# Performance work log

Measured on AMD Instinct MI355X. Metric: run time of the kernel, lower is better.

## Reference

```python
import jax, jax.numpy as jnp
import numpy as np

D_MODEL = 1024
NHEAD = 16
HEAD_DIM = D_MODEL // NHEAD
MASK_FILLER = -1e20


def setup_inputs() -> dict:
    key = jax.random.key(0)
    ks = jax.random.split(key, 8)
    B, S = 2, 2048
    query = jax.random.normal(ks[0], (B, S, D_MODEL), dtype=jnp.float32)
    key_t = jax.random.normal(ks[1], (B, S, D_MODEL), dtype=jnp.float32)
    value = jax.random.normal(ks[2], (B, S, D_MODEL), dtype=jnp.float32)
    mask = jax.random.randint(ks[3], (B, S, S), 0, 2, dtype=jnp.int32)
    # nn.Linear(d_model, d_model, bias=False) weights, shape [out, in]
    scale = 1.0 / np.sqrt(D_MODEL)
    wq = jax.random.uniform(ks[4], (D_MODEL, D_MODEL), jnp.float32, -scale, scale)
    wk = jax.random.uniform(ks[5], (D_MODEL, D_MODEL), jnp.float32, -scale, scale)
    wv = jax.random.uniform(ks[6], (D_MODEL, D_MODEL), jnp.float32, -scale, scale)
    wo = jax.random.uniform(ks[7], (D_MODEL, D_MODEL), jnp.float32, -scale, scale)
    return {"query": query, "key": key_t, "value": value, "mask": mask,
            "wq": wq, "wk": wk, "wv": wv, "wo": wo}


def reference(query, key, value, mask, wq, wk, wv, wo):
    B = query.shape[0]
    # Projections: nn.Linear -> x @ W.T
    q = (query @ wq.T).reshape(B, -1, NHEAD, HEAD_DIM).transpose(0, 2, 1, 3)  # [B,H,Sq,Dh]
    k = (key @ wk.T).reshape(B, -1, NHEAD, HEAD_DIM).transpose(0, 2, 1, 3)    # [B,H,Sk,Dh]
    v = (value @ wv.T).reshape(B, -1, NHEAD, HEAD_DIM).transpose(0, 2, 1, 3)  # [B,H,Sk,Dh]
    scores = jnp.einsum('bhqd,bhkd->bhqk', q, k) / jnp.sqrt(jnp.float32(HEAD_DIM))
    scores = jnp.where(mask[:, None, :, :] == 0, MASK_FILLER, scores)
    attn = jax.nn.softmax(scores, axis=-1)  # dropout p=0.0 -> identity
    out = jnp.einsum('bhqk,bhkd->bhqd', attn, v)  # [B,H,Sq,Dh]
    out = out.transpose(0, 2, 1, 3).reshape(B, -1, D_MODEL)
    return out @ wo.T
```

## Files before the change

### kernel.cpp

```cpp
#include <hip/hip_runtime.h>
#include <stdint.h>

typedef __bf16 bf16x8 __attribute__((ext_vector_type(8)));
typedef __bf16 bf16x4 __attribute__((ext_vector_type(4)));
typedef float floatx4 __attribute__((ext_vector_type(4)));
typedef unsigned short ushort8v __attribute__((ext_vector_type(8)));
typedef unsigned int uint4v __attribute__((ext_vector_type(4)));
typedef unsigned int uint2v __attribute__((ext_vector_type(2)));
typedef unsigned short u16;
typedef unsigned long long u64;

#define GLOAD_LDS16(gp, lp)                                                       \
  __builtin_amdgcn_global_load_lds((__attribute__((address_space(1))) void*)(gp), \
                                   (__attribute__((address_space(3))) void*)(lp), \
                                   16, 0, 0)

__device__ __forceinline__ u16 f2bf(float f) {
  uint32_t u = __builtin_bit_cast(uint32_t, f);
  u = (u + 0x7FFFu + ((u >> 16) & 1u)) >> 16;
  return (u16)u;
}

__device__ __forceinline__ ushort8v load8(const void* base, size_t elemOff, int isf32) {
  if (isf32) {
    const uint32_t* p = (const uint32_t*)base + elemOff;
    uint4v a = *(const uint4v*)p;
    uint4v b = *(const uint4v*)(p + 4);
#pragma unroll
    for (int i = 0; i < 4; ++i) { a[i] += 0x8000u; b[i] += 0x8000u; }
    uint4v r;
    r[0] = __builtin_amdgcn_perm(a[1], a[0], 0x07060302);
    r[1] = __builtin_amdgcn_perm(a[3], a[2], 0x07060302);
    r[2] = __builtin_amdgcn_perm(b[1], b[0], 0x07060302);
    r[3] = __builtin_amdgcn_perm(b[3], b[2], 0x07060302);
    return __builtin_bit_cast(ushort8v, r);
  }
  return *(const ushort8v*)((const u16*)base + elemOff);
}

__global__ void detect_dtype(const u16* __restrict__ q, int* __restrict__ flag) {
  if (threadIdx.x == 0) *flag = 0;
  __syncthreads();
  int hit = 0;
  for (int i = threadIdx.x; i < 8192; i += 256) {
    u16 u = q[i];
    if (((u >> 7) & 0xFF) == 0xFF) hit = 1;
  }
  if (hit) atomicOr(flag, 1);
}

__global__ void pack_mask(const int* __restrict__ mask, u64* __restrict__ mpk) {
  const int gw   = (blockIdx.x * 256 + threadIdx.x) >> 6;
  const int lane = threadIdx.x & 63;
  const int word = gw & 31;
  const int row  = gw >> 5;
  const int m = mask[(size_t)row * 2048 + word * 64 + lane];
  u64 bits = __ballot(m != 0);
  if (lane == 0) mpk[(size_t)row * 32 + word] = bits;
}

__global__ __launch_bounds__(256)
void cvt_all(const void* X0, const void* X1, const void* X2,
             const void* W0, const void* W1, const void* W2, const void* W3,
             u16* __restrict__ Xb, u16* __restrict__ Wb, const int* flagp)
{
  const int isf = *flagp;
  const int id = blockIdx.x;
  const int t  = threadIdx.x;
  const int r2  = t >> 7;
  const int col = (t & 127) * 8;
  const void* src; u16* dst; int row;
  if (id < 6144) {
    const int s = id >> 11;
    src = (s == 0) ? X0 : (s == 1) ? X1 : X2;
    row = (id & 2047) * 2 + r2;
    dst = Xb + (size_t)s * 4096 * 1040 + (size_t)row * 1040 + col;
  } else {
    const int s = (id - 6144) >> 9;
    src = (s == 0) ? W0 : (s == 1) ? W1 : (s == 2) ? W2 : W3;
    row = ((id - 6144) & 511) * 2 + r2;
    dst = Wb + (size_t)s * 1024 * 1040 + (size_t)row * 1040 + col;
  }
  *(ushort8v*)dst = load8(src, (size_t)row * 1024 + col, isf);
}

__global__ __launch_bounds__(256)
void cvt_w(const void* W0, const void* W1, const void* W2, const void* W3,
           u16* __restrict__ dst, const int* flagp) {
  const int isf = *flagp;
  const int z = blockIdx.y;
  const void* src = (z == 0) ? W0 : (z == 1) ? W1 : (z == 2) ? W2 : W3;
  const size_t off = ((size_t)blockIdx.x * 256 + threadIdx.x) * 8;
  *(ushort8v*)(dst + (size_t)z * 1024 * 1024 + off) = load8(src, off, isf);
}

__global__ __launch_bounds__(256, 3)
void gemm_qkv_b(const u16* __restrict__ Xb, const u16* __restrict__ Wb,
                u16* __restrict__ Qb, u16* __restrict__ Kb, u16* __restrict__ Vt)
{
  const int AS = 1040, WS = 1040, N = 1024, K = 1024;
  const int z = blockIdx.z;
  const u16* A = Xb + (size_t)z * 4096 * AS;
  const u16* W = Wb + (size_t)z * 1024 * WS;

  __shared__ __align__(16) u16 lA[2 * 128 * 32];
  __shared__ __align__(16) u16 lB[2 * 128 * 32];

  const int tid  = threadIdx.x;
  const int lane = tid & 63;
  const int quad = lane >> 4;
  const int l15  = lane & 15;
  const int w    = tid >> 6;
  const int wm   = w >> 1, wn = w & 1;
  const int tileM = blockIdx.x * 128;
  const int tileN = blockIdx.y * 128;

  floatx4 acc[4][4] = {};

  const int ldRow = tid >> 2;
  const int ldCol = (tid & 3) * 8;
  const u16* aG = A + (size_t)(tileM + ldRow) * AS + ldCol;
  const u16* bG = W + (size_t)(tileN + ldRow) * WS + ldCol;
  u16* lAp = lA + tid * 8;
  u16* lBp = lB + tid * 8;

  GLOAD_LDS16(aG, lAp);
  GLOAD_LDS16(aG + (size_t)64 * AS, lAp + 2048);
  GLOAD_LDS16(bG, lBp);
  GLOAD_LDS16(bG + (size_t)64 * WS, lBp + 2048);
  __syncthreads();

#pragma unroll 2
  for (int k0 = 0; k0 < K; k0 += 32) {
    const int cur = (k0 >> 5) & 1;
    const int nxo = 4096 * (cur ^ 1);
    if (k0 + 32 < K) {
      GLOAD_LDS16(aG + k0 + 32, lAp + nxo);
      GLOAD_LDS16(aG + (size_t)64 * AS + k0 + 32, lAp + nxo + 2048);
      GLOAD_LDS16(bG + k0 + 32, lBp + nxo);
      GLOAD_LDS16(bG + (size_t)64 * WS + k0 + 32, lBp + nxo + 2048);
    }
    const u16* cA = lA + 4096 * cur;
    const u16* cB = lB + 4096 * cur;
    bf16x8 af[4], bw[4];
#pragma unroll
    for (int i = 0; i < 4; ++i) {
      af[i] = *(const bf16x8*)&cA[(wm * 64 + i * 16 + l15) * 32 + quad * 8];
      bw[i] = *(const bf16x8*)&cB[(wn * 64 + i * 16 + l15) * 32 + quad * 8];
    }
#pragma unroll
    for (int i = 0; i < 4; ++i)
#pragma unroll
      for (int j = 0; j < 4; ++j)
        acc[i][j] = __builtin_amdgcn_mfma_f32_16x16x32_bf16(af[i], bw[j], acc[i][j], 0, 0, 0);
    __syncthreads();
  }

  if (z < 2) {
    u16* C = (z == 0) ? Qb : Kb;
    const float sc = (z == 0) ? 0.18033688011112042f : 1.0f;
#pragma unroll
    for (int i = 0; i < 4; ++i) {
      const int row0 = tileM + wm * 64 + i * 16 + quad * 4;
#pragma unroll
      for (int j = 0; j < 4; ++j) {
        const int col = tileN + wn * 64 + j * 16 + l15;
#pragma unroll
        for (int r = 0; r < 4; ++r)
          C[(size_t)(row0 + r) * N + col] = f2bf(acc[i][j][r] * sc);
      }
    }
  } else {
    const int half = w >> 1;
    u16* myT = (w & 1) ? lB : lA;
#pragma unroll
    for (int pass = 0; pass < 2; ++pass) {
      __syncthreads();
      if (half == pass) {
#pragma unroll
        for (int i = 0; i < 4; ++i)
#pragma unroll
          for (int j = 0; j < 4; ++j)
#pragma unroll
            for (int r = 0; r < 4; ++r) {
              const int lr = i * 16 + quad * 4 + r;
              const int lc = j * 16 + l15;
              myT[lr * 64 + (lc ^ (quad << 4))] = f2bf(acc[i][j][r]);
            }
      }
      __syncthreads();
      if (half == pass) {
        const int n    = lane;
        const int gcol = tileN + wn * 64 + n;
        const int hh = gcol >> 6, dd = gcol & 63;
        const int growBase = tileM + wm * 64;
        const int bb = growBase >> 11;
        const int s0 = growBase & 2047;
        u16* dst = Vt + (((size_t)bb * 16 + hh) * 64 + dd) * 2048 + s0;
#pragma unroll
        for (int m0 = 0; m0 < 64; m0 += 8) {
          ushort8v pk;
#pragma unroll
          for (int t = 0; t < 8; ++t) {
            const int m = m0 + t;
            pk[t] = myT[m * 64 + (n ^ ((m & 12) << 2))];
          }
          *(ushort8v*)(dst + m0) = pk;
        }
      }
    }
  }
}

__global__ __launch_bounds__(256)
void gemm_qkv_f(const void* X0, const void* X1, const void* X2,
                const u16* __restrict__ Wb,
                u16* __restrict__ Qb, u16* __restrict__ Kb, u16* __restrict__ Vt,
                const int* flagp)
{
  const int K = 1024, N = 1024;
  const int isf = *flagp;
  const int z = blockIdx.z;
  const void* A_ = (z == 0) ? X0 : (z == 1) ? X1 : X2;
  const u16* W = Wb + (size_t)z * 1024 * 1024;

  __shared__ __align__(16) u16 lA[128 * 32];
  __shared__ __align__(16) u16 lB[128 * 32];

  const int tid  = threadIdx.x;
  const int lane = tid & 63;
  const int quad = lane >> 4;
  const int l15  = lane & 15;
  const int w    = tid >> 6;
  const int wm   = w >> 1, wn = w & 1;
  const int tileM = blockIdx.x * 128;
  const int tileN = blockIdx.y * 128;

  floatx4 acc[4][4] = {};

  const int ldRow = tid >> 2;
  const int ldCol = (tid & 3) * 8;
  const size_t aOff = (size_t)(tileM + ldRow) * K + ldCol;
  const u16* bG = W + (size_t)(tileN + ldRow) * K + ldCol;
  u16* lAp = lA + tid * 8;
  u16* lBp = lB + tid * 8;

  ushort8v a0 = load8(A_, aOff, isf);
  ushort8v a1 = load8(A_, aOff + (size_t)64 * K, isf);
  ushort8v b0 = *(const ushort8v*)bG;
  ushort8v b1 = *(const ushort8v*)(bG + (size_t)64 * K);

  for (int k0 = 0; k0 < K; k0 += 32) {
    __syncthreads();
    *(ushort8v*)lAp          = a0;
    *(ushort8v*)(lAp + 2048) = a1;
    *(ushort8v*)lBp          = b0;
    *(ushort8v*)(lBp + 2048) = b1;
    __syncthreads();

    if (k0 + 32 < K) {
      a0 = load8(A_, aOff + k0 + 32, isf);
      a1 = load8(A_, aOff + (size_t)64 * K + k0 + 32, isf);
      b0 = *(const ushort8v*)(bG + k0 + 32);
      b1 = *(const ushort8v*)(bG + (size_t)64 * K + k0 + 32);
    }

    bf16x8 af[4], bw[4];
#pragma unroll
    for (int i = 0; i < 4; ++i) {
      af[i] = *(const bf16x8*)&lA[(wm * 64 + i * 16 + l15) * 32 + quad * 8];
      bw[i] = *(const bf16x8*)&lB[(wn * 64 + i * 16 + l15) * 32 + quad * 8];
    }
#pragma unroll
    for (int i = 0; i < 4; ++i)
#pragma unroll
      for (int j = 0; j < 4; ++j)
        acc[i][j] = __builtin_amdgcn_mfma_f32_16x16x32_bf16(af[i], bw[j], acc[i][j], 0, 0, 0);
  }

  if (z < 2) {
    u16* C = (z == 0) ? Qb : Kb;
    const float sc = (z == 0) ? 0.18033688011112042f : 1.0f;
#pragma unroll
    for (int i = 0; i < 4; ++i) {
      const int row0 = tileM + wm * 64 + i * 16 + quad * 4;
#pragma unroll
      for (int j = 0; j < 4; ++j) {
        const int col = tileN + wn * 64 + j * 16 + l15;
#pragma unroll
        for (int r = 0; r < 4; ++r)
          C[(size_t)(row0 + r) * N + col] = f2bf(acc[i][j][r] * sc);
      }
    }
  } else {
    const int half = w >> 1;
    u16* myT = (w & 1) ? lB : lA;
#pragma unroll
    for (int pass = 0; pass < 2; ++pass) {
      __syncthreads();
      if (half == pass) {
#pragma unroll
        for (int i = 0; i < 4; ++i)
#pragma unroll
          for (int j = 0; j < 4; ++j)
#pragma unroll
            for (int r = 0; r < 4; ++r) {
              const int lr = i * 16 + quad * 4 + r;
              const int lc = j * 16 + l15;
              myT[lr * 64 + (lc ^ (quad << 4))] = f2bf(acc[i][j][r]);
            }
      }
      __syncthreads();
      if (half == pass) {
        const int n    = lane;
        const int gcol = tileN + wn * 64 + n;
        const int hh = gcol >> 6, dd = gcol & 63;
        const int growBase = tileM + wm * 64;
        const int bb = growBase >> 11;
        const int s0 = growBase & 2047;
        u16* dst = Vt + (((size_t)bb * 16 + hh) * 64 + dd) * 2048 + s0;
#pragma unroll
        for (int m0 = 0; m0 < 64; m0 += 8) {
          ushort8v pk;
#pragma unroll
          for (int t = 0; t < 8; ++t) {
            const int m = m0 + t;
            pk[t] = myT[m * 64 + (n ^ ((m & 12) << 2))];
          }
          *(ushort8v*)(dst + m0) = pk;
        }
      }
    }
  }
}

__global__ __launch_bounds__(256)
void attn(const u16* Qb, const u16* __restrict__ Kb, const u16* __restrict__ Vt,
          const u64* __restrict__ mpk, u16* AO, int aoStr)
{
  __shared__ __align__(16) u16 lK[2][64 * 64];
  __shared__ __align__(16) u16 lV[2][64 * 64];
  __shared__ __align__(16) u16 lP[4][16 * 64];

  const int tid  = threadIdx.x;
  const int lane = tid & 63;
  const int quad = lane >> 4;
  const int l15  = lane & 15;
  const int w    = tid >> 6;

  const int bh = blockIdx.x;
  const int qt = blockIdx.y;
  const int b  = bh >> 4;
  const int h  = bh & 15;
  const size_t rowB   = (size_t)b * 2048;
  const size_t vtBase = ((size_t)bh * 64) * 2048;

  bf16x8 aq[2];
  {
    const u16* qp = Qb + (rowB + qt * 64 + w * 16 + l15) * 1024 + h * 64 + quad * 8;
    aq[0] = *(const bf16x8*)qp;
    aq[1] = *(const bf16x8*)(qp + 32);
  }

  const ushort8v one_u = {0x3F80, 0x3F80, 0x3F80, 0x3F80, 0x3F80, 0x3F80, 0x3F80, 0x3F80};
  const bf16x8 ones = __builtin_bit_cast(bf16x8, one_u);

  floatx4 o[4], l4;
#pragma unroll
  for (int nb = 0; nb < 4; ++nb) o[nb] = (floatx4){0.f, 0.f, 0.f, 0.f};
  l4 = (floatx4){0.f, 0.f, 0.f, 0.f};

  const u64* mrow = mpk + (rowB + qt * 64 + w * 16 + l15) * 32;
  u16* lPw = &lP[w][0];

  const int r1 = tid >> 3;
  const int cs = ((tid & 7) ^ (r1 & 7)) * 8;
  const u16* kSrc = Kb + (rowB + r1) * 1024 + h * 64 + cs;
  const u16* vSrc = Vt + vtBase + (size_t)r1 * 2048 + cs;

  GLOAD_LDS16(kSrc,                     &lK[0][tid * 8]);
  GLOAD_LDS16(kSrc + (size_t)32 * 1024, &lK[0][tid * 8 + 2048]);
  GLOAD_LDS16(vSrc,                     &lV[0][tid * 8]);
  GLOAD_LDS16(vSrc + (size_t)32 * 2048, &lV[0][tid * 8 + 2048]);

#pragma unroll 2
  for (int kt = 0; kt < 32; ++kt) {
    const int cur = kt & 1;
    __syncthreads();
    if (kt < 31) {
      const u16* kS = kSrc + (size_t)(kt + 1) * 64 * 1024;
      const u16* vS = vSrc + (kt + 1) * 64;
      GLOAD_LDS16(kS,                     &lK[cur ^ 1][tid * 8]);
      GLOAD_LDS16(kS + (size_t)32 * 1024, &lK[cur ^ 1][tid * 8 + 2048]);
      GLOAD_LDS16(vS,                     &lV[cur ^ 1][tid * 8]);
      GLOAD_LDS16(vS + (size_t)32 * 2048, &lV[cur ^ 1][tid * 8 + 2048]);
    }

    const u64 mw = mrow[kt];

#pragma unroll
    for (int nb = 0; nb < 4; ++nb) {
      const int row = nb * 16 + l15;
      const int swk = (row & 7) << 3;
      bf16x8 ak0 = *(const bf16x8*)&lK[cur][row * 64 + ((quad * 8) ^ swk)];
      bf16x8 ak1 = *(const bf16x8*)&lK[cur][row * 64 + ((quad * 8 + 32) ^ swk)];
      floatx4 sacc = {0.f, 0.f, 0.f, 0.f};
      __builtin_amdgcn_s_setprio(1);
      sacc = __builtin_amdgcn_mfma_f32_16x16x32_bf16(ak0, aq[0], sacc, 0, 0, 0);
      sacc = __builtin_amdgcn_mfma_f32_16x16x32_bf16(ak1, aq[1], sacc, 0, 0, 0);
      __builtin_amdgcn_s_setprio(0);
      const uint32_t nib = (uint32_t)(mw >> (nb * 16 + quad * 4)) & 0xFu;
      const float p0 = (nib & 1u) ? __builtin_amdgcn_exp2f(sacc[0]) : 0.0f;
      const float p1 = (nib & 2u) ? __builtin_amdgcn_exp2f(sacc[1]) : 0.0f;
      const float p2 = (nib & 4u) ? __builtin_amdgcn_exp2f(sacc[2]) : 0.0f;
      const float p3 = (nib & 8u) ? __builtin_amdgcn_exp2f(sacc[3]) : 0.0f;
      bf16x4 pk4;
      pk4[0] = (__bf16)p0; pk4[1] = (__bf16)p1;
      pk4[2] = (__bf16)p2; pk4[3] = (__bf16)p3;
      const int col = (nb * 16 + quad * 4) ^ ((l15 & 7) << 3);
      *(bf16x4*)&lPw[l15 * 64 + col] = pk4;
    }

#pragma unroll
    for (int ks = 0; ks < 2; ++ks) {
      bf16x8 ap = *(const bf16x8*)&lPw[l15 * 64 + ((ks * 32 + quad * 8) ^ ((l15 & 7) << 3))];
      bf16x8 bv0 = *(const bf16x8*)&lV[cur][(0 * 16 + l15) * 64 + ((ks * 32 + quad * 8) ^ ((l15 & 7) << 3))];
      bf16x8 bv1 = *(const bf16x8*)&lV[cur][(1 * 16 + l15) * 64 + ((ks * 32 + quad * 8) ^ (((16 + l15) & 7) << 3))];
      bf16x8 bv2 = *(const bf16x8*)&lV[cur][(2 * 16 + l15) * 64 + ((ks * 32 + quad * 8) ^ (((32 + l15) & 7) << 3))];
      bf16x8 bv3 = *(const bf16x8*)&lV[cur][(3 * 16 + l15) * 64 + ((ks * 32 + quad * 8) ^ (((48 + l15) & 7) << 3))];
      __builtin_amdgcn_s_setprio(1);
      o[0] = __builtin_amdgcn_mfma_f32_16x16x32_bf16(ap, bv0, o[0], 0, 0, 0);
      o[1] = __builtin_amdgcn_mfma_f32_16x16x32_bf16(ap, bv1, o[1], 0, 0, 0);
      o[2] = __builtin_amdgcn_mfma_f32_16x16x32_bf16(ap, bv2, o[2], 0, 0, 0);
      o[3] = __builtin_amdgcn_mfma_f32_16x16x32_bf16(ap, bv3, o[3], 0, 0, 0);
      l4 = __builtin_amdgcn_mfma_f32_16x16x32_bf16(ap, ones, l4, 0, 0, 0);
      __builtin_amdgcn_s_setprio(0);
    }
  }

#pragma unroll
  for (int r = 0; r < 4; ++r) {
    const float inv = 1.0f / l4[r];
    const size_t orow = (rowB + qt * 64 + w * 16 + quad * 4 + r) * aoStr + h * 64;
#pragma unroll
    for (int nb = 0; nb < 4; ++nb)
      AO[orow + nb * 16 + l15] = f2bf(o[nb][r] * inv);
  }
}

__global__ __launch_bounds__(256, 3)
void gemm_out(const u16* __restrict__ A, int aStr,
              const u16* __restrict__ W, int wStr, void* C_, const int* flagp)
{
  const int K = 1024, N = 1024;
  const int isf = *flagp;

  __shared__ __align__(16) u16 lA[2 * 64 * 32];
  __shared__ __align__(16) u16 lB[2 * 128 * 32];

  const int tid  = threadIdx.x;
  const int lane = tid & 63;
  const int quad = lane >> 4;
  const int l15  = lane & 15;
  const int w    = tid >> 6;
  const int tileM = blockIdx.x * 64;
  const int tileN = blockIdx.y * 128;

  floatx4 acc[4][2] = {};

  const int ldRow = tid >> 2;
  const int ldCol = (tid & 3) * 8;
  const u16* aG = A + (size_t)(tileM + ldRow) * aStr + ldCol;
  const u16* bG = W + (size_t)(tileN + ldRow) * wStr + ldCol;
  u16* lAp = lA + tid * 8;
  u16* lBp = lB + tid * 8;

  GLOAD_LDS16(aG, lAp);
  GLOAD_LDS16(bG, lBp);
  GLOAD_LDS16(bG + (size_t)64 * wStr, lBp + 2048);
  __syncthreads();

#pragma unroll 2
  for (int k0 = 0; k0 < K; k0 += 32) {
    const int cur = (k0 >> 5) & 1;
    const int nxA = 2048 * (cur ^ 1);
    const int nxB = 4096 * (cur ^ 1);
    if (k0 + 32 < K) {
      GLOAD_LDS16(aG + k0 + 32, lAp + nxA);
      GLOAD_LDS16(bG + k0 + 32, lBp + nxB);
      GLOAD_LDS16(bG + (size_t)64 * wStr + k0 + 32, lBp + nxB + 2048);
    }
    const u16* cA = lA + 2048 * cur;
    const u16* cB = lB + 4096 * cur;
    bf16x8 af[4], bw[2];
#pragma unroll
    for (int i = 0; i < 4; ++i)
      af[i] = *(const bf16x8*)&cA[(i * 16 + l15) * 32 + quad * 8];
#pragma unroll
    for (int j = 0; j < 2; ++j)
      bw[j] = *(const bf16x8*)&cB[(w * 32 + j * 16 + l15) * 32 + quad * 8];
#pragma unroll
    for (int i = 0; i < 4; ++i)
#pragma unroll
      for (int j = 0; j < 2; ++j)
        acc[i][j] = __builtin_amdgcn_mfma_f32_16x16x32_bf16(af[i], bw[j], acc[i][j], 0, 0, 0);
    __syncthreads();
  }

#pragma unroll
  for (int i = 0; i < 4; ++i) {
    const int row0 = tileM + i * 16 + quad * 4;
#pragma unroll
    for (int j = 0; j < 2; ++j) {
      const int col = tileN + w * 32 + j * 16 + l15;
#pragma unroll
      for (int r = 0; r < 4; ++r) {
        const size_t off = (size_t)(row0 + r) * N + col;
        if (isf) ((float*)C_)[off] = acc[i][j][r];
        else     ((u16*)C_)[off]   = f2bf(acc[i][j][r]);
      }
    }
  }
}

extern "C" void kernel_launch(void* const* d_in, const int* in_sizes, int n_in,
                              void* d_out, int out_size, void* d_ws, size_t ws_size,
                              hipStream_t stream)
{
  const int* mk = (const int*)d_in[3];

  int* flag = (int*)d_ws;
  u64* mpk  = (u64*)((char*)d_ws + 256);
  const size_t SZ = (size_t)4096 * 1024;
  u16* Qb = (u16*)((char*)d_ws + 256 + (size_t)1048576);
  u16* Kb = Qb + SZ;
  u16* Vt = Kb + SZ;
  u16* Wb = Vt + SZ;

  const size_t WB_PAD = (size_t)4 * 1024 * 1040;
  const size_t XB_PAD = (size_t)3 * 4096 * 1040;
  const size_t NEED = 256 + 1048576 + 3 * SZ * 2 + WB_PAD * 2 + XB_PAD * 2;

  detect_dtype<<<1, 256, 0, stream>>>((const u16*)d_in[0], flag);
  pack_mask<<<32768, 256, 0, stream>>>(mk, mpk);

  if (ws_size >= NEED) {
    u16* Xb = Wb + WB_PAD;
    cvt_all<<<8192, 256, 0, stream>>>(d_in[0], d_in[1], d_in[2],
                                      d_in[4], d_in[5], d_in[6], d_in[7],
                                      Xb, Wb, flag);
    gemm_qkv_b<<<dim3(32, 8, 3), 256, 0, stream>>>(Xb, Wb, Qb, Kb, Vt);
    u16* AOp = Xb;
    attn<<<dim3(32, 32), 256, 0, stream>>>(Qb, Kb, Vt, mpk, AOp, 1040);
    gemm_out<<<dim3(64, 8), 256, 0, stream>>>(AOp, 1040,
                                              Wb + (size_t)3 * 1024 * 1040, 1040,
                                              d_out, flag);
  } else {
    cvt_w<<<dim3(512, 4), 256, 0, stream>>>(d_in[4], d_in[5], d_in[6], d_in[7], Wb, flag);
    gemm_qkv_f<<<dim3(32, 8, 3), 256, 0, stream>>>(d_in[0], d_in[1], d_in[2],
                                                   Wb, Qb, Kb, Vt, flag);
    attn<<<dim3(32, 32), 256, 0, stream>>>(Qb, Kb, Vt, mpk, Qb, 1024);
    gemm_out<<<dim3(64, 8), 256, 0, stream>>>(Qb, 1024,
                                              Wb + (size_t)3 * 1024 * 1024, 1024,
                                              d_out, flag);
  }
}
```

Baseline: 279.9 us.

## Split attention key tiles across two wave groups and reduce partials in LDS

```diff
diff --git a/kernel.cpp b/kernel.cpp
--- a/kernel.cpp
+++ b/kernel.cpp
@@ -6,7 +6,6 @@
 typedef float floatx4 __attribute__((ext_vector_type(4)));
 typedef unsigned short ushort8v __attribute__((ext_vector_type(8)));
 typedef unsigned int uint4v __attribute__((ext_vector_type(4)));
-typedef unsigned int uint2v __attribute__((ext_vector_type(2)));
 typedef unsigned short u16;
 typedef unsigned long long u64;
 
@@ -334,19 +333,21 @@
   }
 }
 
-__global__ __launch_bounds__(256)
+__global__ __launch_bounds__(512, 8)
 void attn(const u16* Qb, const u16* __restrict__ Kb, const u16* __restrict__ Vt,
           const u64* __restrict__ mpk, u16* AO, int aoStr)
 {
   __shared__ __align__(16) u16 lK[2][64 * 64];
   __shared__ __align__(16) u16 lV[2][64 * 64];
-  __shared__ __align__(16) u16 lP[4][16 * 64];
+  __shared__ __align__(16) u16 lP[8][16 * 32];
 
   const int tid  = threadIdx.x;
   const int lane = tid & 63;
   const int quad = lane >> 4;
   const int l15  = lane & 15;
   const int w    = tid >> 6;
+  const int qg   = w & 3;
+  const int kh   = w >> 2;
 
   const int bh = blockIdx.x;
   const int qt = blockIdx.y;
@@ -357,7 +358,7 @@
 
   bf16x8 aq[2];
   {
-    const u16* qp = Qb + (rowB + qt * 64 + w * 16 + l15) * 1024 + h * 64 + quad * 8;
+    const u16* qp = Qb + (rowB + qt * 64 + qg * 16 + l15) * 1024 + h * 64 + quad * 8;
     aq[0] = *(const bf16x8*)qp;
     aq[1] = *(const bf16x8*)(qp + 32);
   }
@@ -370,7 +371,7 @@
   for (int nb = 0; nb < 4; ++nb) o[nb] = (floatx4){0.f, 0.f, 0.f, 0.f};
   l4 = (floatx4){0.f, 0.f, 0.f, 0.f};
 
-  const u64* mrow = mpk + (rowB + qt * 64 + w * 16 + l15) * 32;
+  const uint32_t* mrow32 = (const uint32_t*)(mpk + (rowB + qt * 64 + qg * 16 + l15) * 32);
   u16* lPw = &lP[w][0];
 
   const int r1 = tid >> 3;
@@ -378,38 +379,30 @@
   const u16* kSrc = Kb + (rowB + r1) * 1024 + h * 64 + cs;
   const u16* vSrc = Vt + vtBase + (size_t)r1 * 2048 + cs;
 
-  GLOAD_LDS16(kSrc,                     &lK[0][tid * 8]);
-  GLOAD_LDS16(kSrc + (size_t)32 * 1024, &lK[0][tid * 8 + 2048]);
-  GLOAD_LDS16(vSrc,                     &lV[0][tid * 8]);
-  GLOAD_LDS16(vSrc + (size_t)32 * 2048, &lV[0][tid * 8 + 2048]);
+  GLOAD_LDS16(kSrc, &lK[0][tid * 8]);
+  GLOAD_LDS16(vSrc, &lV[0][tid * 8]);
 
 #pragma unroll 2
   for (int kt = 0; kt < 32; ++kt) {
     const int cur = kt & 1;
     __syncthreads();
     if (kt < 31) {
-      const u16* kS = kSrc + (size_t)(kt + 1) * 64 * 1024;
-      const u16* vS = vSrc + (kt + 1) * 64;
-      GLOAD_LDS16(kS,                     &lK[cur ^ 1][tid * 8]);
-      GLOAD_LDS16(kS + (size_t)32 * 1024, &lK[cur ^ 1][tid * 8 + 2048]);
-      GLOAD_LDS16(vS,                     &lV[cur ^ 1][tid * 8]);
-      GLOAD_LDS16(vS + (size_t)32 * 2048, &lV[cur ^ 1][tid * 8 + 2048]);
-    }
-
-    const u64 mw = mrow[kt];
-
-#pragma unroll
-    for (int nb = 0; nb < 4; ++nb) {
-      const int row = nb * 16 + l15;
+      GLOAD_LDS16(kSrc + (size_t)(kt + 1) * 64 * 1024, &lK[cur ^ 1][tid * 8]);
+      GLOAD_LDS16(vSrc + (kt + 1) * 64,                &lV[cur ^ 1][tid * 8]);
+    }
+
+    const uint32_t mw32 = mrow32[kt * 2 + kh];
+
+#pragma unroll
+    for (int nb2 = 0; nb2 < 2; ++nb2) {
+      const int row = kh * 32 + nb2 * 16 + l15;
       const int swk = (row & 7) << 3;
       bf16x8 ak0 = *(const bf16x8*)&lK[cur][row * 64 + ((quad * 8) ^ swk)];
       bf16x8 ak1 = *(const bf16x8*)&lK[cur][row * 64 + ((quad * 8 + 32) ^ swk)];
       floatx4 sacc = {0.f, 0.f, 0.f, 0.f};
-      __builtin_amdgcn_s_setprio(1);
       sacc = __builtin_amdgcn_mfma_f32_16x16x32_bf16(ak0, aq[0], sacc, 0, 0, 0);
       sacc = __builtin_amdgcn_mfma_f32_16x16x32_bf16(ak1, aq[1], sacc, 0, 0, 0);
-      __builtin_amdgcn_s_setprio(0);
-      const uint32_t nib = (uint32_t)(mw >> (nb * 16 + quad * 4)) & 0xFu;
+      const uint32_t nib = (mw32 >> (nb2 * 16 + quad * 4)) & 0xFu;
       const float p0 = (nib & 1u) ? __builtin_amdgcn_exp2f(sacc[0]) : 0.0f;
       const float p1 = (nib & 2u) ? __builtin_amdgcn_exp2f(sacc[1]) : 0.0f;
       const float p2 = (nib & 4u) ? __builtin_amdgcn_exp2f(sacc[2]) : 0.0f;
@@ -417,34 +410,45 @@
       bf16x4 pk4;
       pk4[0] = (__bf16)p0; pk4[1] = (__bf16)p1;
       pk4[2] = (__bf16)p2; pk4[3] = (__bf16)p3;
-      const int col = (nb * 16 + quad * 4) ^ ((l15 & 7) << 3);
-      *(bf16x4*)&lPw[l15 * 64 + col] = pk4;
-    }
-
-#pragma unroll
-    for (int ks = 0; ks < 2; ++ks) {
-      bf16x8 ap = *(const bf16x8*)&lPw[l15 * 64 + ((ks * 32 + quad * 8) ^ ((l15 & 7) << 3))];
-      bf16x8 bv0 = *(const bf16x8*)&lV[cur][(0 * 16 + l15) * 64 + ((ks * 32 + quad * 8) ^ ((l15 & 7) << 3))];
-      bf16x8 bv1 = *(const bf16x8*)&lV[cur][(1 * 16 + l15) * 64 + ((ks * 32 + quad * 8) ^ (((16 + l15) & 7) << 3))];
-      bf16x8 bv2 = *(const bf16x8*)&lV[cur][(2 * 16 + l15) * 64 + ((ks * 32 + quad * 8) ^ (((32 + l15) & 7) << 3))];
-      bf16x8 bv3 = *(const bf16x8*)&lV[cur][(3 * 16 + l15) * 64 + ((ks * 32 + quad * 8) ^ (((48 + l15) & 7) << 3))];
-      __builtin_amdgcn_s_setprio(1);
-      o[0] = __builtin_amdgcn_mfma_f32_16x16x32_bf16(ap, bv0, o[0], 0, 0, 0);
-      o[1] = __builtin_amdgcn_mfma_f32_16x16x32_bf16(ap, bv1, o[1], 0, 0, 0);
-      o[2] = __builtin_amdgcn_mfma_f32_16x16x32_bf16(ap, bv2, o[2], 0, 0, 0);
-      o[3] = __builtin_amdgcn_mfma_f32_16x16x32_bf16(ap, bv3, o[3], 0, 0, 0);
-      l4 = __builtin_amdgcn_mfma_f32_16x16x32_bf16(ap, ones, l4, 0, 0, 0);
-      __builtin_amdgcn_s_setprio(0);
-    }
-  }
-
-#pragma unroll
-  for (int r = 0; r < 4; ++r) {
-    const float inv = 1.0f / l4[r];
-    const size_t orow = (rowB + qt * 64 + w * 16 + quad * 4 + r) * aoStr + h * 64;
+      const int col = (nb2 * 16 + quad * 4) ^ ((l15 & 3) << 3);
+      *(bf16x4*)&lPw[l15 * 32 + col] = pk4;
+    }
+
+    bf16x8 ap = *(const bf16x8*)&lPw[l15 * 32 + ((quad * 8) ^ ((l15 & 3) << 3))];
+#pragma unroll
+    for (int nb = 0; nb < 4; ++nb) {
+      const int row = nb * 16 + l15;
+      bf16x8 bv = *(const bf16x8*)&lV[cur][row * 64 + ((kh * 32 + quad * 8) ^ ((row & 7) << 3))];
+      o[nb] = __builtin_amdgcn_mfma_f32_16x16x32_bf16(ap, bv, o[nb], 0, 0, 0);
+    }
+    l4 = __builtin_amdgcn_mfma_f32_16x16x32_bf16(ap, ones, l4, 0, 0, 0);
+  }
+
+  __syncthreads();
+  float* so = (float*)&lK[0][0];
+  float* sl = (float*)&lV[0][0];
+  if (kh == 1) {
+    const int base = (qg * 64 + lane) * 16;
+    const int lb   = (qg * 64 + lane) * 4;
 #pragma unroll
     for (int nb = 0; nb < 4; ++nb)
-      AO[orow + nb * 16 + l15] = f2bf(o[nb][r] * inv);
+#pragma unroll
+      for (int r = 0; r < 4; ++r) so[base + nb * 4 + r] = o[nb][r];
+#pragma unroll
+    for (int r = 0; r < 4; ++r) sl[lb + r] = l4[r];
+  }
+  __syncthreads();
+  if (kh == 0) {
+    const int base = (qg * 64 + lane) * 16;
+    const int lb   = (qg * 64 + lane) * 4;
+#pragma unroll
+    for (int r = 0; r < 4; ++r) {
+      const float inv = 1.0f / (l4[r] + sl[lb + r]);
+      const size_t orow = (rowB + qt * 64 + qg * 16 + quad * 4 + r) * aoStr + h * 64;
+#pragma unroll
+      for (int nb = 0; nb < 4; ++nb)
+        AO[orow + nb * 16 + l15] = f2bf((o[nb][r] + so[base + nb * 4 + r]) * inv);
+    }
   }
 }
 
@@ -551,7 +555,7 @@
                                       Xb, Wb, flag);
     gemm_qkv_b<<<dim3(32, 8, 3), 256, 0, stream>>>(Xb, Wb, Qb, Kb, Vt);
     u16* AOp = Xb;
-    attn<<<dim3(32, 32), 256, 0, stream>>>(Qb, Kb, Vt, mpk, AOp, 1040);
+    attn<<<dim3(32, 32), 512, 0, stream>>>(Qb, Kb, Vt, mpk, AOp, 1040);
     gemm_out<<<dim3(64, 8), 256, 0, stream>>>(AOp, 1040,
                                               Wb + (size_t)3 * 1024 * 1040, 1040,
                                               d_out, flag);
@@ -559,7 +563,7 @@
     cvt_w<<<dim3(512, 4), 256, 0, stream>>>(d_in[4], d_in[5], d_in[6], d_in[7], Wb, flag);
     gemm_qkv_f<<<dim3(32, 8, 3), 256, 0, stream>>>(d_in[0], d_in[1], d_in[2],
                                                    Wb, Qb, Kb, Vt, flag);
-    attn<<<dim3(32, 32), 256, 0, stream>>>(Qb, Kb, Vt, mpk, Qb, 1024);
+    attn<<<dim3(32, 32), 512, 0, stream>>>(Qb, Kb, Vt, mpk, Qb, 1024);
     gemm_out<<<dim3(64, 8), 256, 0, stream>>>(Qb, 1024,
                                               Wb + (size_t)3 * 1024 * 1024, 1024,
                                               d_out, flag);
```

New measurement: 285.0 us. Within noise of the previous version (+1.8%).
